# Optimization experiments

Measured on AMD Instinct MI355X. Metric: run time of the kernel, lower is better.

The kernel has to match this reference:

```python
import jax, jax.numpy as jnp
import numpy as np

N = 100000
E = 1600000
F_IN = 512
H1, C1 = 8, 8      # layer-1: 8 heads, 8 dims each (concat -> 64)
H2, C2 = 1, 16     # layer-2: 1 head, num_classes=16
SLOPE = 0.2        # GATConv leaky_relu negative slope


def setup_inputs() -> dict:
    key = jax.random.key(0)
    ks = jax.random.split(key, 10)
    x = jax.random.normal(ks[0], (N, F_IN), dtype=jnp.float32)
    edge_index = jax.random.randint(ks[1], (2, E), 0, N, dtype=jnp.int32)
    s = 0.05
    W1 = jax.random.normal(ks[2], (F_IN, H1 * C1), dtype=jnp.float32) * s
    a1_src = jax.random.normal(ks[3], (H1, C1), dtype=jnp.float32) * s
    a1_dst = jax.random.normal(ks[4], (H1, C1), dtype=jnp.float32) * s
    b1 = jnp.zeros((H1 * C1,), dtype=jnp.float32)
    W2 = jax.random.normal(ks[5], (H1 * C1, H2 * C2), dtype=jnp.float32) * s
    a2_src = jax.random.normal(ks[6], (H2, C2), dtype=jnp.float32) * s
    a2_dst = jax.random.normal(ks[7], (H2, C2), dtype=jnp.float32) * s
    b2 = jnp.zeros((H2 * C2,), dtype=jnp.float32)
    return {"x": x, "edge_index": edge_index, "W1": W1, "a1_src": a1_src,
            "a1_dst": a1_dst, "b1": b1, "W2": W2, "a2_src": a2_src,
            "a2_dst": a2_dst, "b2": b2}


def _gat_conv(h, src, dst, W, a_src, a_dst, b, heads, ch):
    n = h.shape[0]
    hp = (h @ W).reshape(n, heads, ch)                      # [N,H,C]
    al_s = jnp.einsum('nhc,hc->nh', hp, a_src)              # [N,H]
    al_d = jnp.einsum('nhc,hc->nh', hp, a_dst)              # [N,H]
    e = jax.nn.leaky_relu(al_s[src] + al_d[dst], SLOPE)     # [E,H]
    # segment softmax over edges sharing a destination (self-loops guarantee >=1 edge/node)
    emax = jax.lax.stop_gradient(jax.ops.segment_max(e, dst, num_segments=n))
    ee = jnp.exp(e - emax[dst])
    denom = jax.ops.segment_sum(ee, dst, num_segments=n)
    alpha = ee / denom[dst]                                 # [E,H]
    msg = hp[src] * alpha[:, :, None]                       # [E,H,C]
    out = jax.ops.segment_sum(msg, dst, num_segments=n)     # [N,H,C]
    return out.reshape(n, heads * ch) + b


def reference(x, edge_index, W1, a1_src, a1_dst, b1, W2, a2_src, a2_dst, b2):
    n = x.shape[0]
    loops = jnp.arange(n, dtype=edge_index.dtype)           # add_self_loops=True
    src = jnp.concatenate([edge_index[0], loops])
    dst = jnp.concatenate([edge_index[1], loops])
    h = jax.nn.elu(_gat_conv(x, src, dst, W1, a1_src, a1_dst, b1, H1, C1))
    h = _gat_conv(h, src, dst, W2, a2_src, a2_dst, b2, H2, C2)
    return jax.nn.log_softmax(h, axis=1)
```

## Files before the change

### kernel.cpp

```cpp
#include <hip/hip_runtime.h>
#include <hip/hip_bf16.h>

#define N_NODES 100000
#define F_IN    512
#define H1      8
#define C1      8
#define D1      64
#define C2      16
#define SLOPE   0.2f
#define CAP     48
#define PSHIFT  9
#define PPART   196
#define CAPP    9216
#define CHUNK   4096

typedef __bf16 bf16_t;
typedef bf16_t bf16x8 __attribute__((ext_vector_type(8)));
typedef float  f32x4  __attribute__((ext_vector_type(4)));

__global__ __launch_bounds__(256) void part_kernel(
    const float* __restrict__ W1, bf16_t* __restrict__ W1b,
    const int* __restrict__ ei, int* __restrict__ pcnt, int2* __restrict__ pfifo,
    int E, int total)
{
    __shared__ int hist[PPART];
    __shared__ int lofs[PPART];
    __shared__ int gbase[PPART];
    __shared__ int cursor[PPART];
    __shared__ int sdata[256];
    __shared__ int2 fifo[CHUNK];

    const int t = threadIdx.x;
    const int chunk0 = (int)blockIdx.x * CHUNK;

    for (int i = (int)blockIdx.x * 256 + t; i < 64 * 512; i += (int)gridDim.x * 256) {
        int nn = i >> 9, k = i & 511;
        W1b[i] = (bf16_t)W1[k * 64 + nn];
    }

    for (int i = t; i < PPART; i += 256) hist[i] = 0;
    __syncthreads();

    int srcs[16], dsts[16];
    const int e0 = chunk0 + t * 16;
    if (e0 + 16 <= E) {
#pragma unroll
        for (int q = 0; q < 4; ++q) {
            int4 s = *(const int4*)(ei + e0 + q * 4);
            int4 d = *(const int4*)(ei + E + e0 + q * 4);
            srcs[q*4+0]=s.x; srcs[q*4+1]=s.y; srcs[q*4+2]=s.z; srcs[q*4+3]=s.w;
            dsts[q*4+0]=d.x; dsts[q*4+1]=d.y; dsts[q*4+2]=d.z; dsts[q*4+3]=d.w;
        }
    } else {
#pragma unroll
        for (int j = 0; j < 16; ++j) {
            int e = e0 + j;
            if (e < E)          { srcs[j] = ei[e]; dsts[j] = ei[E + e]; }
            else if (e < total) { srcs[j] = dsts[j] = e - E; }
            else                { srcs[j] = -1;    dsts[j] = -1; }
        }
    }
#pragma unroll
    for (int j = 0; j < 16; ++j)
        if (dsts[j] >= 0) atomicAdd(&hist[dsts[j] >> PSHIFT], 1);
    __syncthreads();

    int hv = (t < PPART) ? hist[t] : 0;
    sdata[t] = hv;
    __syncthreads();
    for (int off = 1; off < 256; off <<= 1) {
        int x = (t >= off) ? sdata[t - off] : 0;
        __syncthreads();
        sdata[t] += x;
        __syncthreads();
    }
    if (t < PPART) {
        int lo = sdata[t] - hv;
        lofs[t]   = lo;
        cursor[t] = lo;
        gbase[t]  = hv ? atomicAdd(&pcnt[t], hv) : 0;
    }
    __syncthreads();

#pragma unroll
    for (int j = 0; j < 16; ++j) {
        if (dsts[j] >= 0) {
            int p = dsts[j] >> PSHIFT;
            int slot = atomicAdd(&cursor[p], 1);
            fifo[slot] = make_int2(srcs[j], dsts[j]);
        }
    }
    __syncthreads();

    const int w = t >> 6, lane = t & 63;
    for (int p = w; p < PPART; p += 4) {
        int len = hist[p];
        int lo  = lofs[p];
        int gb  = gbase[p];
        int2* dstp = pfifo + (size_t)p * CAPP;
        for (int j = lane; j < len; j += 64) {
            int g = gb + j;
            if (g < CAPP) dstp[g] = fifo[lo + j];
        }
    }
}

__global__ __launch_bounds__(512) void place_kernel(
    const int2* __restrict__ pfifo, const int* __restrict__ pcnt,
    int* __restrict__ buckets, int* __restrict__ cnt, int n)
{
    __shared__ int lcnt[1 << PSHIFT];
    const int p = blockIdx.x;
    const int dbase = p << PSHIFT;
    const int nd = min(1 << PSHIFT, n - dbase);
    const int t = threadIdx.x;
    for (int i = t; i < nd; i += 512) lcnt[i] = 0;
    __syncthreads();

    int len = pcnt[p]; if (len > CAPP) len = CAPP;
    const int2* f = pfifo + (size_t)p * CAPP;

    int i = t;
    for (; i + 1536 < len; i += 2048) {
        int2 e0 = f[i], e1 = f[i + 512], e2 = f[i + 1024], e3 = f[i + 1536];
        int s0 = atomicAdd(&lcnt[e0.y - dbase], 1);
        int s1 = atomicAdd(&lcnt[e1.y - dbase], 1);
        int s2 = atomicAdd(&lcnt[e2.y - dbase], 1);
        int s3 = atomicAdd(&lcnt[e3.y - dbase], 1);
        if (s0 < CAP) buckets[(size_t)e0.y * CAP + s0] = e0.x;
        if (s1 < CAP) buckets[(size_t)e1.y * CAP + s1] = e1.x;
        if (s2 < CAP) buckets[(size_t)e2.y * CAP + s2] = e2.x;
        if (s3 < CAP) buckets[(size_t)e3.y * CAP + s3] = e3.x;
    }
    for (; i < len; i += 512) {
        int2 e = f[i];
        int s = atomicAdd(&lcnt[e.y - dbase], 1);
        if (s < CAP) buckets[(size_t)e.y * CAP + s] = e.x;
    }
    __syncthreads();
    for (int i2 = t; i2 < nd; i2 += 512) cnt[dbase + i2] = min(lcnt[i2], CAP);
}

__global__ __launch_bounds__(512, 4) void gemm1_kernel(
    const float* __restrict__ X, const bf16_t* __restrict__ Bt,
    const float* __restrict__ a1s, const float* __restrict__ a1d,
    bf16_t* __restrict__ HPb, float* __restrict__ als1, float* __restrict__ ald1,
    int n)
{
    __shared__ __align__(16) bf16_t Bsm[8 * 4 * 64 * 8];

    const int t = threadIdx.x;
    const int rowbase = (int)blockIdx.x * 128;
    const int w = t >> 6;
    const int lane = t & 63;

    const int rloc = lane & 15;
    const int koff = (lane >> 4) * 8;

    int grow = rowbase + w * 16 + rloc;
    int growc = (grow < n) ? grow : (n - 1);
    const float* arow = X + (size_t)growc * F_IN + koff;

    f32x4 acc[4];
#pragma unroll
    for (int nt = 0; nt < 4; ++nt) acc[nt] = (f32x4){0.f, 0.f, 0.f, 0.f};

#pragma unroll
    for (int half = 0; half < 2; ++half) {
        for (int i = t; i < 2048; i += 512) {
            int l9 = i & 63;
            int nt = (i >> 6) & 3;
            int ks = i >> 8;
            int row = nt * 16 + (l9 & 15);
            int col = (half * 8 + ks) * 32 + (l9 >> 4) * 8;
            *(bf16x8*)(Bsm + (size_t)i * 8) =
                *(const bf16x8*)(Bt + (size_t)row * F_IN + col);
        }
        __syncthreads();

#pragma unroll 4
        for (int ks = 0; ks < 8; ++ks) {
            int kg = (half * 8 + ks) * 32;
            float4 xa0 = *(const float4*)(arow + kg);
            float4 xa1 = *(const float4*)(arow + kg + 4);
            bf16x8 af;
            af[0]=(bf16_t)xa0.x; af[1]=(bf16_t)xa0.y; af[2]=(bf16_t)xa0.z; af[3]=(bf16_t)xa0.w;
            af[4]=(bf16_t)xa1.x; af[5]=(bf16_t)xa1.y; af[6]=(bf16_t)xa1.z; af[7]=(bf16_t)xa1.w;
#pragma unroll
            for (int nt = 0; nt < 4; ++nt) {
                bf16x8 b = *(const bf16x8*)(Bsm + ((ks * 4 + nt) * 64 + lane) * 8);
                acc[nt] = __builtin_amdgcn_mfma_f32_16x16x32_bf16(af, b, acc[nt], 0, 0, 0);
            }
        }
        __syncthreads();
    }

    const int colg = lane & 15;
    const int quad = lane >> 4;
    const int b    = colg >> 3;
    float cs[4], cd[4];
#pragma unroll
    for (int nt = 0; nt < 4; ++nt) {
        cs[nt] = a1s[nt * 16 + colg];
        cd[nt] = a1d[nt * 16 + colg];
    }

#pragma unroll
    for (int i = 0; i < 4; ++i) {
        int r = rowbase + w * 16 + quad * 4 + i;
        bool ok = r < n;
        if (ok) {
            bf16_t* hr = HPb + (size_t)r * D1;
            hr[colg]      = (bf16_t)acc[0][i];
            hr[16 + colg] = (bf16_t)acc[1][i];
            hr[32 + colg] = (bf16_t)acc[2][i];
            hr[48 + colg] = (bf16_t)acc[3][i];
        }
#pragma unroll
        for (int nt = 0; nt < 4; ++nt) {
            float ps = acc[nt][i] * cs[nt];
            float pd = acc[nt][i] * cd[nt];
            ps += __shfl_xor(ps, 1, 64);  pd += __shfl_xor(pd, 1, 64);
            ps += __shfl_xor(ps, 2, 64);  pd += __shfl_xor(pd, 2, 64);
            ps += __shfl_xor(ps, 4, 64);  pd += __shfl_xor(pd, 4, 64);
            if (ok && (colg & 7) == 0) {
                als1[(size_t)r * 8 + 2 * nt + b] = ps;
                ald1[(size_t)r * 8 + 2 * nt + b] = pd;
            }
        }
    }
}

__global__ __launch_bounds__(256) void agg1_kernel(
    const bf16_t* __restrict__ hp1,
    const float* __restrict__ als, const float* __restrict__ ald,
    const int* __restrict__ cnt, const int* __restrict__ buckets,
    const float* __restrict__ b1,
    const float* __restrict__ W2,
    const float* __restrict__ a2s, const float* __restrict__ a2d,
    bf16_t* __restrict__ HP2b, float* __restrict__ als2, float* __restrict__ ald2,
    int n)
{
    __shared__ float Wsm[64 * 17];
    const int t = threadIdx.x;
    for (int i = t; i < 1024; i += 256)
        Wsm[(i >> 4) * 17 + (i & 15)] = W2[i];
    __syncthreads();

    int node = blockIdx.x * 4 + (t >> 6);
    if (node >= n) return;
    int lane = t & 63;
    int h = lane >> 3;

    int m = cnt[node]; if (m > CAP) m = CAP;
    const int* bp = buckets + (size_t)node * CAP;
    float ad = ald[node * 8 + h];
    float den = 0.f, acc = 0.f;

    int i = 0;
    for (; i + 8 <= m; i += 8) {
        int s0 = bp[i + 0], s1 = bp[i + 1], s2 = bp[i + 2], s3 = bp[i + 3];
        int s4 = bp[i + 4], s5 = bp[i + 5], s6 = bp[i + 6], s7 = bp[i + 7];
        float a0 = als[s0 * 8 + h], a1 = als[s1 * 8 + h];
        float a2 = als[s2 * 8 + h], a3 = als[s3 * 8 + h];
        float a4 = als[s4 * 8 + h], a5 = als[s5 * 8 + h];
        float a6 = als[s6 * 8 + h], a7 = als[s7 * 8 + h];
        float v0 = (float)hp1[(size_t)s0 * D1 + lane];
        float v1 = (float)hp1[(size_t)s1 * D1 + lane];
        float v2 = (float)hp1[(size_t)s2 * D1 + lane];
        float v3 = (float)hp1[(size_t)s3 * D1 + lane];
        float v4 = (float)hp1[(size_t)s4 * D1 + lane];
        float v5 = (float)hp1[(size_t)s5 * D1 + lane];
        float v6 = (float)hp1[(size_t)s6 * D1 + lane];
        float v7 = (float)hp1[(size_t)s7 * D1 + lane];
        float e0 = a0 + ad; e0 = (e0 > 0.f) ? e0 : SLOPE * e0;
        float e1 = a1 + ad; e1 = (e1 > 0.f) ? e1 : SLOPE * e1;
        float e2 = a2 + ad; e2 = (e2 > 0.f) ? e2 : SLOPE * e2;
        float e3 = a3 + ad; e3 = (e3 > 0.f) ? e3 : SLOPE * e3;
        float e4 = a4 + ad; e4 = (e4 > 0.f) ? e4 : SLOPE * e4;
        float e5 = a5 + ad; e5 = (e5 > 0.f) ? e5 : SLOPE * e5;
        float e6 = a6 + ad; e6 = (e6 > 0.f) ? e6 : SLOPE * e6;
        float e7 = a7 + ad; e7 = (e7 > 0.f) ? e7 : SLOPE * e7;
        float w0 = __expf(e0), w1 = __expf(e1), w2 = __expf(e2), w3 = __expf(e3);
        float w4 = __expf(e4), w5 = __expf(e5), w6 = __expf(e6), w7 = __expf(e7);
        den += ((w0 + w1) + (w2 + w3)) + ((w4 + w5) + (w6 + w7));
        acc = fmaf(w0, v0, acc);
        acc = fmaf(w1, v1, acc);
        acc = fmaf(w2, v2, acc);
        acc = fmaf(w3, v3, acc);
        acc = fmaf(w4, v4, acc);
        acc = fmaf(w5, v5, acc);
        acc = fmaf(w6, v6, acc);
        acc = fmaf(w7, v7, acc);
    }
    for (; i < m; ++i) {
        int s = bp[i];
        float e = als[s * 8 + h] + ad;
        e = (e > 0.f) ? e : SLOPE * e;
        float ee = __expf(e);
        den += ee;
        acc = fmaf(ee, (float)hp1[(size_t)s * D1 + lane], acc);
    }
    float v = acc / den + b1[lane];
    v = (v > 0.f) ? v : (__expf(v) - 1.f);

    const int g = lane >> 4, c = lane & 15;
    float o = 0.f;
#pragma unroll
    for (int kk = 0; kk < 16; ++kk) {
        float hk = __shfl(v, g * 16 + kk, 64);
        o = fmaf(hk, Wsm[(g * 16 + kk) * 17 + c], o);
    }
    o += __shfl_xor(o, 16, 64);
    o += __shfl_xor(o, 32, 64);
    if (g == 0) HP2b[(size_t)node * 16 + c] = (bf16_t)o;

    float rs = o * a2s[c];
    float rd = o * a2d[c];
    rs += __shfl_xor(rs, 1, 64);  rd += __shfl_xor(rd, 1, 64);
    rs += __shfl_xor(rs, 2, 64);  rd += __shfl_xor(rd, 2, 64);
    rs += __shfl_xor(rs, 4, 64);  rd += __shfl_xor(rd, 4, 64);
    rs += __shfl_xor(rs, 8, 64);  rd += __shfl_xor(rd, 8, 64);
    if (lane == 0) { als2[node] = rs; ald2[node] = rd; }
}

__global__ __launch_bounds__(256) void agg2_kernel(
    const bf16_t* __restrict__ hp2,
    const float* __restrict__ als, const float* __restrict__ ald,
    const int* __restrict__ cnt, const int* __restrict__ buckets,
    const float* __restrict__ b2,
    float* __restrict__ out, int n)
{
    int node = blockIdx.x * 16 + (threadIdx.x >> 4);
    if (node >= n) return;
    int c = threadIdx.x & 15;

    int m0c = cnt[node]; if (m0c > CAP) m0c = CAP;
    const int* bp = buckets + (size_t)node * CAP;
    float ad = ald[node];
    float den = 0.f, acc = 0.f;

    int i = 0;
    for (; i + 8 <= m0c; i += 8) {
        int s0 = bp[i + 0], s1 = bp[i + 1], s2 = bp[i + 2], s3 = bp[i + 3];
        int s4 = bp[i + 4], s5 = bp[i + 5], s6 = bp[i + 6], s7 = bp[i + 7];
        float a0 = als[s0], a1 = als[s1], a2 = als[s2], a3 = als[s3];
        float a4 = als[s4], a5 = als[s5], a6 = als[s6], a7 = als[s7];
        float v0 = (float)hp2[(size_t)s0 * 16 + c];
        float v1 = (float)hp2[(size_t)s1 * 16 + c];
        float v2 = (float)hp2[(size_t)s2 * 16 + c];
        float v3 = (float)hp2[(size_t)s3 * 16 + c];
        float v4 = (float)hp2[(size_t)s4 * 16 + c];
        float v5 = (float)hp2[(size_t)s5 * 16 + c];
        float v6 = (float)hp2[(size_t)s6 * 16 + c];
        float v7 = (float)hp2[(size_t)s7 * 16 + c];
        float e0 = a0 + ad; e0 = (e0 > 0.f) ? e0 : SLOPE * e0;
        float e1 = a1 + ad; e1 = (e1 > 0.f) ? e1 : SLOPE * e1;
        float e2 = a2 + ad; e2 = (e2 > 0.f) ? e2 : SLOPE * e2;
        float e3 = a3 + ad; e3 = (e3 > 0.f) ? e3 : SLOPE * e3;
        float e4 = a4 + ad; e4 = (e4 > 0.f) ? e4 : SLOPE * e4;
        float e5 = a5 + ad; e5 = (e5 > 0.f) ? e5 : SLOPE * e5;
        float e6 = a6 + ad; e6 = (e6 > 0.f) ? e6 : SLOPE * e6;
        float e7 = a7 + ad; e7 = (e7 > 0.f) ? e7 : SLOPE * e7;
        float w0 = __expf(e0), w1 = __expf(e1), w2 = __expf(e2), w3 = __expf(e3);
        float w4 = __expf(e4), w5 = __expf(e5), w6 = __expf(e6), w7 = __expf(e7);
        den += ((w0 + w1) + (w2 + w3)) + ((w4 + w5) + (w6 + w7));
        acc = fmaf(w0, v0, acc);
        acc = fmaf(w1, v1, acc);
        acc = fmaf(w2, v2, acc);
        acc = fmaf(w3, v3, acc);
        acc = fmaf(w4, v4, acc);
        acc = fmaf(w5, v5, acc);
        acc = fmaf(w6, v6, acc);
        acc = fmaf(w7, v7, acc);
    }
    for (; i < m0c; ++i) {
        int s = bp[i];
        float e = als[s] + ad;
        e = (e > 0.f) ? e : SLOPE * e;
        float ee = __expf(e);
        den += ee;
        acc = fmaf(ee, (float)hp2[(size_t)s * 16 + c], acc);
    }
    float v = acc / den + b2[c];

    float m = v;
    m = fmaxf(m, __shfl_xor(m, 8, 16));
    m = fmaxf(m, __shfl_xor(m, 4, 16));
    m = fmaxf(m, __shfl_xor(m, 2, 16));
    m = fmaxf(m, __shfl_xor(m, 1, 16));
    float ex = __expf(v - m);
    float sum = ex;
    sum += __shfl_xor(sum, 8, 16);
    sum += __shfl_xor(sum, 4, 16);
    sum += __shfl_xor(sum, 2, 16);
    sum += __shfl_xor(sum, 1, 16);
    out[(size_t)node * 16 + c] = v - m - __logf(sum);
}

extern "C" void kernel_launch(void* const* d_in, const int* in_sizes, int n_in,
                              void* d_out, int out_size, void* d_ws, size_t ws_size,
                              hipStream_t stream)
{
    const float* x      = (const float*)d_in[0];
    const int*   ei     = (const int*)  d_in[1];
    const float* W1     = (const float*)d_in[2];
    const float* a1_src = (const float*)d_in[3];
    const float* a1_dst = (const float*)d_in[4];
    const float* b1     = (const float*)d_in[5];
    const float* W2     = (const float*)d_in[6];
    const float* a2_src = (const float*)d_in[7];
    const float* a2_dst = (const float*)d_in[8];
    const float* b2     = (const float*)d_in[9];
    float* out = (float*)d_out;

    const int N = in_sizes[0] / F_IN;
    const int E = in_sizes[1] / 2;
    const int TOT = E + N;

    char* base = (char*)d_ws;
    size_t off = 0;
    auto carve = [&](size_t bytes) -> char* {
        char* p = base + off;
        off += (bytes + 255) & ~(size_t)255;
        return p;
    };
    bf16_t* hp1b    = (bf16_t*)carve((size_t)N * D1 * 2);
    float*  h1      = (float*) carve((size_t)N * D1 * 4);
    bf16_t* hp2b    = (bf16_t*)carve((size_t)N * 16 * 2);
    float*  als1    = (float*) carve((size_t)N * 8 * 4);
    float*  ald1    = (float*) carve((size_t)N * 8 * 4);
    float*  als2    = (float*) carve((size_t)N * 4);
    float*  ald2    = (float*) carve((size_t)N * 4);
    int*    cnt     = (int*)   carve((size_t)N * 4);
    int*    pcnt    = (int*)   carve((size_t)PPART * 4);
    int*    buckets = (int*)   carve((size_t)N * CAP * 4);
    bf16_t* W1b     = (bf16_t*)carve((size_t)64 * 512 * 2);
    int2*  pfifo   = (int2*)h1;

    const int Gp = (TOT + CHUNK - 1) / CHUNK;

    hipMemsetAsync(pcnt, 0, (size_t)PPART * 4, stream);

    part_kernel<<<Gp, 256, 0, stream>>>(W1, W1b, ei, pcnt, pfifo, E, TOT);
    place_kernel<<<PPART, 512, 0, stream>>>(pfifo, pcnt, buckets, cnt, N);

    gemm1_kernel<<<(N + 127) / 128, 512, 0, stream>>>(x, W1b, a1_src, a1_dst,
                                                      hp1b, als1, ald1, N);

    agg1_kernel<<<(N + 3) / 4, 256, 0, stream>>>(hp1b, als1, ald1, cnt, buckets,
                                                 b1, W2, a2_src, a2_dst,
                                                 hp2b, als2, ald2, N);

    agg2_kernel<<<(N + 15) / 16, 256, 0, stream>>>(hp2b, als2, ald2, cnt, buckets, b2, out, N);
}
```

Before: 507.9 us.

## Merge place and GEMM kernels into one launch; split agg1 edges across wave pairs

The bucket placement work and the layer-1 GEMM now share a single launch, with the first PPART blocks doing placement and the rest doing GEMM rows. The two independent stages can then overlap on the GPU, and one launch gap goes away. agg1 now uses 512 threads, with two waves per node splitting the 8-edge groups and combining partial sums through shared memory. This doubles memory-level parallelism for the gather at the cost of a block-wide sync and shared-memory traffic, and the merged kernel's shared-memory footprint rises.

```diff
diff --git a/kernel.cpp b/kernel.cpp
--- a/kernel.cpp
+++ b/kernel.cpp
@@ -105,52 +105,52 @@
     }
 }
 
-__global__ __launch_bounds__(512) void place_kernel(
+__global__ __launch_bounds__(512, 4) void pg_kernel(
     const int2* __restrict__ pfifo, const int* __restrict__ pcnt,
-    int* __restrict__ buckets, int* __restrict__ cnt, int n)
-{
-    __shared__ int lcnt[1 << PSHIFT];
-    const int p = blockIdx.x;
-    const int dbase = p << PSHIFT;
-    const int nd = min(1 << PSHIFT, n - dbase);
-    const int t = threadIdx.x;
-    for (int i = t; i < nd; i += 512) lcnt[i] = 0;
-    __syncthreads();
-
-    int len = pcnt[p]; if (len > CAPP) len = CAPP;
-    const int2* f = pfifo + (size_t)p * CAPP;
-
-    int i = t;
-    for (; i + 1536 < len; i += 2048) {
-        int2 e0 = f[i], e1 = f[i + 512], e2 = f[i + 1024], e3 = f[i + 1536];
-        int s0 = atomicAdd(&lcnt[e0.y - dbase], 1);
-        int s1 = atomicAdd(&lcnt[e1.y - dbase], 1);
-        int s2 = atomicAdd(&lcnt[e2.y - dbase], 1);
-        int s3 = atomicAdd(&lcnt[e3.y - dbase], 1);
-        if (s0 < CAP) buckets[(size_t)e0.y * CAP + s0] = e0.x;
-        if (s1 < CAP) buckets[(size_t)e1.y * CAP + s1] = e1.x;
-        if (s2 < CAP) buckets[(size_t)e2.y * CAP + s2] = e2.x;
-        if (s3 < CAP) buckets[(size_t)e3.y * CAP + s3] = e3.x;
-    }
-    for (; i < len; i += 512) {
-        int2 e = f[i];
-        int s = atomicAdd(&lcnt[e.y - dbase], 1);
-        if (s < CAP) buckets[(size_t)e.y * CAP + s] = e.x;
-    }
-    __syncthreads();
-    for (int i2 = t; i2 < nd; i2 += 512) cnt[dbase + i2] = min(lcnt[i2], CAP);
-}
-
-__global__ __launch_bounds__(512, 4) void gemm1_kernel(
+    int* __restrict__ buckets, int* __restrict__ cnt,
     const float* __restrict__ X, const bf16_t* __restrict__ Bt,
     const float* __restrict__ a1s, const float* __restrict__ a1d,
     bf16_t* __restrict__ HPb, float* __restrict__ als1, float* __restrict__ ald1,
     int n)
 {
+    __shared__ int lcnt[1 << PSHIFT];
     __shared__ __align__(16) bf16_t Bsm[8 * 4 * 64 * 8];
 
     const int t = threadIdx.x;
-    const int rowbase = (int)blockIdx.x * 128;
+
+    if (blockIdx.x < PPART) {
+        const int p = blockIdx.x;
+        const int dbase = p << PSHIFT;
+        const int nd = min(1 << PSHIFT, n - dbase);
+        for (int i = t; i < nd; i += 512) lcnt[i] = 0;
+        __syncthreads();
+
+        int len = pcnt[p]; if (len > CAPP) len = CAPP;
+        const int2* f = pfifo + (size_t)p * CAPP;
+
+        int i = t;
+        for (; i + 1536 < len; i += 2048) {
+            int2 e0 = f[i], e1 = f[i + 512], e2 = f[i + 1024], e3 = f[i + 1536];
+            int s0 = atomicAdd(&lcnt[e0.y - dbase], 1);
+            int s1 = atomicAdd(&lcnt[e1.y - dbase], 1);
+            int s2 = atomicAdd(&lcnt[e2.y - dbase], 1);
+            int s3 = atomicAdd(&lcnt[e3.y - dbase], 1);
+            if (s0 < CAP) buckets[(size_t)e0.y * CAP + s0] = e0.x;
+            if (s1 < CAP) buckets[(size_t)e1.y * CAP + s1] = e1.x;
+            if (s2 < CAP) buckets[(size_t)e2.y * CAP + s2] = e2.x;
+            if (s3 < CAP) buckets[(size_t)e3.y * CAP + s3] = e3.x;
+        }
+        for (; i < len; i += 512) {
+            int2 e = f[i];
+            int s = atomicAdd(&lcnt[e.y - dbase], 1);
+            if (s < CAP) buckets[(size_t)e.y * CAP + s] = e.x;
+        }
+        __syncthreads();
+        for (int i2 = t; i2 < nd; i2 += 512) cnt[dbase + i2] = min(lcnt[i2], CAP);
+        return;
+    }
+
+    const int rowbase = ((int)blockIdx.x - PPART) * 128;
     const int w = t >> 6;
     const int lane = t & 63;
 
@@ -231,7 +231,7 @@
     }
 }
 
-__global__ __launch_bounds__(256) void agg1_kernel(
+__global__ __launch_bounds__(512) void agg1_kernel(
     const bf16_t* __restrict__ hp1,
     const float* __restrict__ als, const float* __restrict__ ald,
     const int* __restrict__ cnt, const int* __restrict__ buckets,
@@ -242,25 +242,33 @@
     int n)
 {
     __shared__ float Wsm[64 * 17];
+    __shared__ float sacc[8][64];
+    __shared__ float sden[8][64];
+
     const int t = threadIdx.x;
-    for (int i = t; i < 1024; i += 256)
+    for (int i = t; i < 1024; i += 512)
         Wsm[(i >> 4) * 17 + (i & 15)] = W2[i];
-    __syncthreads();
-
-    int node = blockIdx.x * 4 + (t >> 6);
-    if (node >= n) return;
-    int lane = t & 63;
-    int h = lane >> 3;
-
-    int m = cnt[node]; if (m > CAP) m = CAP;
-    const int* bp = buckets + (size_t)node * CAP;
-    float ad = ald[node * 8 + h];
+
+    const int wv   = t >> 6;
+    const int pair = wv & 1;
+    const int slot = wv >> 1;
+    const int lane = t & 63;
+    const int h    = lane >> 3;
+
+    int node  = blockIdx.x * 4 + slot;
+    bool valid = node < n;
+    int nodec = valid ? node : (n - 1);
+
+    int m = cnt[nodec]; if (m > CAP) m = CAP;
+    const int* bp = buckets + (size_t)nodec * CAP;
+    float ad = ald[nodec * 8 + h];
     float den = 0.f, acc = 0.f;
 
-    int i = 0;
-    for (; i + 8 <= m; i += 8) {
-        int s0 = bp[i + 0], s1 = bp[i + 1], s2 = bp[i + 2], s3 = bp[i + 3];
-        int s4 = bp[i + 4], s5 = bp[i + 5], s6 = bp[i + 6], s7 = bp[i + 7];
+    const int G = m >> 3;
+    for (int g = pair; g < G; g += 2) {
+        const int base = g * 8;
+        int s0 = bp[base + 0], s1 = bp[base + 1], s2 = bp[base + 2], s3 = bp[base + 3];
+        int s4 = bp[base + 4], s5 = bp[base + 5], s6 = bp[base + 6], s7 = bp[base + 7];
         float a0 = als[s0 * 8 + h], a1 = als[s1 * 8 + h];
         float a2 = als[s2 * 8 + h], a3 = als[s3 * 8 + h];
         float a4 = als[s4 * 8 + h], a5 = als[s5 * 8 + h];
@@ -293,35 +301,46 @@
         acc = fmaf(w6, v6, acc);
         acc = fmaf(w7, v7, acc);
     }
-    for (; i < m; ++i) {
-        int s = bp[i];
-        float e = als[s * 8 + h] + ad;
-        e = (e > 0.f) ? e : SLOPE * e;
-        float ee = __expf(e);
-        den += ee;
-        acc = fmaf(ee, (float)hp1[(size_t)s * D1 + lane], acc);
-    }
-    float v = acc / den + b1[lane];
-    v = (v > 0.f) ? v : (__expf(v) - 1.f);
-
-    const int g = lane >> 4, c = lane & 15;
-    float o = 0.f;
-#pragma unroll
-    for (int kk = 0; kk < 16; ++kk) {
-        float hk = __shfl(v, g * 16 + kk, 64);
-        o = fmaf(hk, Wsm[(g * 16 + kk) * 17 + c], o);
-    }
-    o += __shfl_xor(o, 16, 64);
-    o += __shfl_xor(o, 32, 64);
-    if (g == 0) HP2b[(size_t)node * 16 + c] = (bf16_t)o;
-
-    float rs = o * a2s[c];
-    float rd = o * a2d[c];
-    rs += __shfl_xor(rs, 1, 64);  rd += __shfl_xor(rd, 1, 64);
-    rs += __shfl_xor(rs, 2, 64);  rd += __shfl_xor(rd, 2, 64);
-    rs += __shfl_xor(rs, 4, 64);  rd += __shfl_xor(rd, 4, 64);
-    rs += __shfl_xor(rs, 8, 64);  rd += __shfl_xor(rd, 8, 64);
-    if (lane == 0) { als2[node] = rs; ald2[node] = rd; }
+    if (pair == (G & 1)) {
+        for (int i = G * 8; i < m; ++i) {
+            int s = bp[i];
+            float e = als[s * 8 + h] + ad;
+            e = (e > 0.f) ? e : SLOPE * e;
+            float ee = __expf(e);
+            den += ee;
+            acc = fmaf(ee, (float)hp1[(size_t)s * D1 + lane], acc);
+        }
+    }
+
+    sacc[wv][lane] = acc;
+    sden[wv][lane] = den;
+    __syncthreads();
+
+    if (pair == 0) {
+        acc += sacc[wv ^ 1][lane];
+        den += sden[wv ^ 1][lane];
+        float v = acc / den + b1[lane];
+        v = (v > 0.f) ? v : (__expf(v) - 1.f);
+
+        const int g2 = lane >> 4, c = lane & 15;
+        float o = 0.f;
+#pragma unroll
+        for (int kk = 0; kk < 16; ++kk) {
+            float hk = __shfl(v, g2 * 16 + kk, 64);
+            o = fmaf(hk, Wsm[(g2 * 16 + kk) * 17 + c], o);
+        }
+        o += __shfl_xor(o, 16, 64);
+        o += __shfl_xor(o, 32, 64);
+        if (valid && g2 == 0) HP2b[(size_t)node * 16 + c] = (bf16_t)o;
+
+        float rs = o * a2s[c];
+        float rd = o * a2d[c];
+        rs += __shfl_xor(rs, 1, 64);  rd += __shfl_xor(rd, 1, 64);
+        rs += __shfl_xor(rs, 2, 64);  rd += __shfl_xor(rd, 2, 64);
+        rs += __shfl_xor(rs, 4, 64);  rd += __shfl_xor(rd, 4, 64);
+        rs += __shfl_xor(rs, 8, 64);  rd += __shfl_xor(rd, 8, 64);
+        if (valid && lane == 0) { als2[node] = rs; ald2[node] = rd; }
+    }
 }
 
 __global__ __launch_bounds__(256) void agg2_kernel(
@@ -439,16 +458,17 @@
     int2*  pfifo   = (int2*)h1;
 
     const int Gp = (TOT + CHUNK - 1) / CHUNK;
+    const int Gg = (N + 127) / 128;
 
     hipMemsetAsync(pcnt, 0, (size_t)PPART * 4, stream);
 
     part_kernel<<<Gp, 256, 0, stream>>>(W1, W1b, ei, pcnt, pfifo, E, TOT);
-    place_kernel<<<PPART, 512, 0, stream>>>(pfifo, pcnt, buckets, cnt, N);
-
-    gemm1_kernel<<<(N + 127) / 128, 512, 0, stream>>>(x, W1b, a1_src, a1_dst,
-                                                      hp1b, als1, ald1, N);
-
-    agg1_kernel<<<(N + 3) / 4, 256, 0, stream>>>(hp1b, als1, ald1, cnt, buckets,
+
+    pg_kernel<<<PPART + Gg, 512, 0, stream>>>(pfifo, pcnt, buckets, cnt,
+                                              x, W1b, a1_src, a1_dst,
+                                              hp1b, als1, ald1, N);
+
+    agg1_kernel<<<(N + 3) / 4, 512, 0, stream>>>(hp1b, als1, ald1, cnt, buckets,
                                                  b1, W2, a2_src, a2_dst,
                                                  hp2b, als2, ald2, N);
 
```

Result: slower. 588.1 us (+15.8%).

## Fuse bucket placement with GEMM1 launch and batch-gather aggregation neighbors

Applied to the files above, without the earlier changes.

Merges place_kernel and gemm1_kernel into one launch. The first PPART blocks do the bucket placement and the remaining blocks do the GEMM, so the placement work can overlap the GEMM and one launch gap goes away. The two aggregation kernels now load all 48 bucket indices with vector int4 loads into registers. They then issue 16 independent gathers per section, masking out-of-range edges, which raises memory-level parallelism. This costs more registers (the occupancy hint is set to 6) and adds wasted gathers of node 0 for padded slots.

```diff
diff --git a/kernel.cpp b/kernel.cpp
--- a/kernel.cpp
+++ b/kernel.cpp
@@ -105,52 +105,52 @@
     }
 }
 
-__global__ __launch_bounds__(512) void place_kernel(
+__global__ __launch_bounds__(512, 4) void pg_kernel(
     const int2* __restrict__ pfifo, const int* __restrict__ pcnt,
-    int* __restrict__ buckets, int* __restrict__ cnt, int n)
-{
-    __shared__ int lcnt[1 << PSHIFT];
-    const int p = blockIdx.x;
-    const int dbase = p << PSHIFT;
-    const int nd = min(1 << PSHIFT, n - dbase);
-    const int t = threadIdx.x;
-    for (int i = t; i < nd; i += 512) lcnt[i] = 0;
-    __syncthreads();
-
-    int len = pcnt[p]; if (len > CAPP) len = CAPP;
-    const int2* f = pfifo + (size_t)p * CAPP;
-
-    int i = t;
-    for (; i + 1536 < len; i += 2048) {
-        int2 e0 = f[i], e1 = f[i + 512], e2 = f[i + 1024], e3 = f[i + 1536];
-        int s0 = atomicAdd(&lcnt[e0.y - dbase], 1);
-        int s1 = atomicAdd(&lcnt[e1.y - dbase], 1);
-        int s2 = atomicAdd(&lcnt[e2.y - dbase], 1);
-        int s3 = atomicAdd(&lcnt[e3.y - dbase], 1);
-        if (s0 < CAP) buckets[(size_t)e0.y * CAP + s0] = e0.x;
-        if (s1 < CAP) buckets[(size_t)e1.y * CAP + s1] = e1.x;
-        if (s2 < CAP) buckets[(size_t)e2.y * CAP + s2] = e2.x;
-        if (s3 < CAP) buckets[(size_t)e3.y * CAP + s3] = e3.x;
-    }
-    for (; i < len; i += 512) {
-        int2 e = f[i];
-        int s = atomicAdd(&lcnt[e.y - dbase], 1);
-        if (s < CAP) buckets[(size_t)e.y * CAP + s] = e.x;
-    }
-    __syncthreads();
-    for (int i2 = t; i2 < nd; i2 += 512) cnt[dbase + i2] = min(lcnt[i2], CAP);
-}
-
-__global__ __launch_bounds__(512, 4) void gemm1_kernel(
+    int* __restrict__ buckets, int* __restrict__ cnt,
     const float* __restrict__ X, const bf16_t* __restrict__ Bt,
     const float* __restrict__ a1s, const float* __restrict__ a1d,
     bf16_t* __restrict__ HPb, float* __restrict__ als1, float* __restrict__ ald1,
     int n)
 {
+    __shared__ int lcnt[1 << PSHIFT];
     __shared__ __align__(16) bf16_t Bsm[8 * 4 * 64 * 8];
 
     const int t = threadIdx.x;
-    const int rowbase = (int)blockIdx.x * 128;
+
+    if (blockIdx.x < PPART) {
+        const int p = blockIdx.x;
+        const int dbase = p << PSHIFT;
+        const int nd = min(1 << PSHIFT, n - dbase);
+        for (int i = t; i < nd; i += 512) lcnt[i] = 0;
+        __syncthreads();
+
+        int len = pcnt[p]; if (len > CAPP) len = CAPP;
+        const int2* f = pfifo + (size_t)p * CAPP;
+
+        int i = t;
+        for (; i + 1536 < len; i += 2048) {
+            int2 e0 = f[i], e1 = f[i + 512], e2 = f[i + 1024], e3 = f[i + 1536];
+            int s0 = atomicAdd(&lcnt[e0.y - dbase], 1);
+            int s1 = atomicAdd(&lcnt[e1.y - dbase], 1);
+            int s2 = atomicAdd(&lcnt[e2.y - dbase], 1);
+            int s3 = atomicAdd(&lcnt[e3.y - dbase], 1);
+            if (s0 < CAP) buckets[(size_t)e0.y * CAP + s0] = e0.x;
+            if (s1 < CAP) buckets[(size_t)e1.y * CAP + s1] = e1.x;
+            if (s2 < CAP) buckets[(size_t)e2.y * CAP + s2] = e2.x;
+            if (s3 < CAP) buckets[(size_t)e3.y * CAP + s3] = e3.x;
+        }
+        for (; i < len; i += 512) {
+            int2 e = f[i];
+            int s = atomicAdd(&lcnt[e.y - dbase], 1);
+            if (s < CAP) buckets[(size_t)e.y * CAP + s] = e.x;
+        }
+        __syncthreads();
+        for (int i2 = t; i2 < nd; i2 += 512) cnt[dbase + i2] = min(lcnt[i2], CAP);
+        return;
+    }
+
+    const int rowbase = ((int)blockIdx.x - PPART) * 128;
     const int w = t >> 6;
     const int lane = t & 63;
 
@@ -231,7 +231,27 @@
     }
 }
 
-__global__ __launch_bounds__(256) void agg1_kernel(
+#define AGG1_SEC(G0)                                                        \
+    {                                                                       \
+        float a_[16], v_[16];                                               \
+        _Pragma("unroll")                                                   \
+        for (int j = 0; j < 16; ++j) {                                      \
+            int s = (G0 + j < m) ? idx[G0 + j] : 0;                         \
+            a_[j] = als[s * 8 + h];                                         \
+            v_[j] = (float)hp1[(size_t)s * D1 + lane];                      \
+        }                                                                   \
+        _Pragma("unroll")                                                   \
+        for (int j = 0; j < 16; ++j) {                                      \
+            float e = a_[j] + ad;                                           \
+            e = (e > 0.f) ? e : SLOPE * e;                                  \
+            float wgt = __expf(e);                                          \
+            if (G0 + j >= m) wgt = 0.f;                                     \
+            den += wgt;                                                     \
+            acc = fmaf(wgt, v_[j], acc);                                    \
+        }                                                                   \
+    }
+
+__global__ __launch_bounds__(256, 6) void agg1_kernel(
     const bf16_t* __restrict__ hp1,
     const float* __restrict__ als, const float* __restrict__ ald,
     const int* __restrict__ cnt, const int* __restrict__ buckets,
@@ -255,65 +275,32 @@
     int m = cnt[node]; if (m > CAP) m = CAP;
     const int* bp = buckets + (size_t)node * CAP;
     float ad = ald[node * 8 + h];
+
+    int idx[48];
+#pragma unroll
+    for (int q = 0; q < 12; ++q) {
+        int4 v4 = *(const int4*)(bp + q * 4);
+        idx[q*4+0] = v4.x; idx[q*4+1] = v4.y; idx[q*4+2] = v4.z; idx[q*4+3] = v4.w;
+    }
+
     float den = 0.f, acc = 0.f;
-
-    int i = 0;
-    for (; i + 8 <= m; i += 8) {
-        int s0 = bp[i + 0], s1 = bp[i + 1], s2 = bp[i + 2], s3 = bp[i + 3];
-        int s4 = bp[i + 4], s5 = bp[i + 5], s6 = bp[i + 6], s7 = bp[i + 7];
-        float a0 = als[s0 * 8 + h], a1 = als[s1 * 8 + h];
-        float a2 = als[s2 * 8 + h], a3 = als[s3 * 8 + h];
-        float a4 = als[s4 * 8 + h], a5 = als[s5 * 8 + h];
-        float a6 = als[s6 * 8 + h], a7 = als[s7 * 8 + h];
-        float v0 = (float)hp1[(size_t)s0 * D1 + lane];
-        float v1 = (float)hp1[(size_t)s1 * D1 + lane];
-        float v2 = (float)hp1[(size_t)s2 * D1 + lane];
-        float v3 = (float)hp1[(size_t)s3 * D1 + lane];
-        float v4 = (float)hp1[(size_t)s4 * D1 + lane];
-        float v5 = (float)hp1[(size_t)s5 * D1 + lane];
-        float v6 = (float)hp1[(size_t)s6 * D1 + lane];
-        float v7 = (float)hp1[(size_t)s7 * D1 + lane];
-        float e0 = a0 + ad; e0 = (e0 > 0.f) ? e0 : SLOPE * e0;
-        float e1 = a1 + ad; e1 = (e1 > 0.f) ? e1 : SLOPE * e1;
-        float e2 = a2 + ad; e2 = (e2 > 0.f) ? e2 : SLOPE * e2;
-        float e3 = a3 + ad; e3 = (e3 > 0.f) ? e3 : SLOPE * e3;
-        float e4 = a4 + ad; e4 = (e4 > 0.f) ? e4 : SLOPE * e4;
-        float e5 = a5 + ad; e5 = (e5 > 0.f) ? e5 : SLOPE * e5;
-        float e6 = a6 + ad; e6 = (e6 > 0.f) ? e6 : SLOPE * e6;
-        float e7 = a7 + ad; e7 = (e7 > 0.f) ? e7 : SLOPE * e7;
-        float w0 = __expf(e0), w1 = __expf(e1), w2 = __expf(e2), w3 = __expf(e3);
-        float w4 = __expf(e4), w5 = __expf(e5), w6 = __expf(e6), w7 = __expf(e7);
-        den += ((w0 + w1) + (w2 + w3)) + ((w4 + w5) + (w6 + w7));
-        acc = fmaf(w0, v0, acc);
-        acc = fmaf(w1, v1, acc);
-        acc = fmaf(w2, v2, acc);
-        acc = fmaf(w3, v3, acc);
-        acc = fmaf(w4, v4, acc);
-        acc = fmaf(w5, v5, acc);
-        acc = fmaf(w6, v6, acc);
-        acc = fmaf(w7, v7, acc);
-    }
-    for (; i < m; ++i) {
-        int s = bp[i];
-        float e = als[s * 8 + h] + ad;
-        e = (e > 0.f) ? e : SLOPE * e;
-        float ee = __expf(e);
-        den += ee;
-        acc = fmaf(ee, (float)hp1[(size_t)s * D1 + lane], acc);
-    }
+    AGG1_SEC(0);
+    if (m > 16) AGG1_SEC(16);
+    if (m > 32) AGG1_SEC(32);
+
     float v = acc / den + b1[lane];
     v = (v > 0.f) ? v : (__expf(v) - 1.f);
 
-    const int g = lane >> 4, c = lane & 15;
+    const int g2 = lane >> 4, c = lane & 15;
     float o = 0.f;
 #pragma unroll
     for (int kk = 0; kk < 16; ++kk) {
-        float hk = __shfl(v, g * 16 + kk, 64);
-        o = fmaf(hk, Wsm[(g * 16 + kk) * 17 + c], o);
+        float hk = __shfl(v, g2 * 16 + kk, 64);
+        o = fmaf(hk, Wsm[(g2 * 16 + kk) * 17 + c], o);
     }
     o += __shfl_xor(o, 16, 64);
     o += __shfl_xor(o, 32, 64);
-    if (g == 0) HP2b[(size_t)node * 16 + c] = (bf16_t)o;
+    if (g2 == 0) HP2b[(size_t)node * 16 + c] = (bf16_t)o;
 
     float rs = o * a2s[c];
     float rd = o * a2d[c];
@@ -324,7 +311,27 @@
     if (lane == 0) { als2[node] = rs; ald2[node] = rd; }
 }
 
-__global__ __launch_bounds__(256) void agg2_kernel(
+#define AGG2_SEC(G0)                                                        \
+    {                                                                       \
+        float a_[16], v_[16];                                               \
+        _Pragma("unroll")                                                   \
+        for (int j = 0; j < 16; ++j) {                                      \
+            int s = (G0 + j < m) ? idx[G0 + j] : 0;                         \
+            a_[j] = als[s];                                                 \
+            v_[j] = (float)hp2[(size_t)s * 16 + c];                         \
+        }                                                                   \
+        _Pragma("unroll")                                                   \
+        for (int j = 0; j < 16; ++j) {                                      \
+            float e = a_[j] + ad;                                           \
+            e = (e > 0.f) ? e : SLOPE * e;                                  \
+            float wgt = __expf(e);                                          \
+            if (G0 + j >= m) wgt = 0.f;                                     \
+            den += wgt;                                                     \
+            acc = fmaf(wgt, v_[j], acc);                                    \
+        }                                                                   \
+    }
+
+__global__ __launch_bounds__(256, 6) void agg2_kernel(
     const bf16_t* __restrict__ hp2,
     const float* __restrict__ als, const float* __restrict__ ald,
     const int* __restrict__ cnt, const int* __restrict__ buckets,
@@ -335,67 +342,36 @@
     if (node >= n) return;
     int c = threadIdx.x & 15;
 
-    int m0c = cnt[node]; if (m0c > CAP) m0c = CAP;
+    int m = cnt[node]; if (m > CAP) m = CAP;
     const int* bp = buckets + (size_t)node * CAP;
     float ad = ald[node];
+
+    int idx[48];
+#pragma unroll
+    for (int q = 0; q < 12; ++q) {
+        int4 v4 = *(const int4*)(bp + q * 4);
+        idx[q*4+0] = v4.x; idx[q*4+1] = v4.y; idx[q*4+2] = v4.z; idx[q*4+3] = v4.w;
+    }
+
     float den = 0.f, acc = 0.f;
-
-    int i = 0;
-    for (; i + 8 <= m0c; i += 8) {
-        int s0 = bp[i + 0], s1 = bp[i + 1], s2 = bp[i + 2], s3 = bp[i + 3];
-        int s4 = bp[i + 4], s5 = bp[i + 5], s6 = bp[i + 6], s7 = bp[i + 7];
-        float a0 = als[s0], a1 = als[s1], a2 = als[s2], a3 = als[s3];
-        float a4 = als[s4], a5 = als[s5], a6 = als[s6], a7 = als[s7];
-        float v0 = (float)hp2[(size_t)s0 * 16 + c];
-        float v1 = (float)hp2[(size_t)s1 * 16 + c];
-        float v2 = (float)hp2[(size_t)s2 * 16 + c];
-        float v3 = (float)hp2[(size_t)s3 * 16 + c];
-        float v4 = (float)hp2[(size_t)s4 * 16 + c];
-        float v5 = (float)hp2[(size_t)s5 * 16 + c];
-        float v6 = (float)hp2[(size_t)s6 * 16 + c];
-        float v7 = (float)hp2[(size_t)s7 * 16 + c];
-        float e0 = a0 + ad; e0 = (e0 > 0.f) ? e0 : SLOPE * e0;
-        float e1 = a1 + ad; e1 = (e1 > 0.f) ? e1 : SLOPE * e1;
-        float e2 = a2 + ad; e2 = (e2 > 0.f) ? e2 : SLOPE * e2;
-        float e3 = a3 + ad; e3 = (e3 > 0.f) ? e3 : SLOPE * e3;
-        float e4 = a4 + ad; e4 = (e4 > 0.f) ? e4 : SLOPE * e4;
-        float e5 = a5 + ad; e5 = (e5 > 0.f) ? e5 : SLOPE * e5;
-        float e6 = a6 + ad; e6 = (e6 > 0.f) ? e6 : SLOPE * e6;
-        float e7 = a7 + ad; e7 = (e7 > 0.f) ? e7 : SLOPE * e7;
-        float w0 = __expf(e0), w1 = __expf(e1), w2 = __expf(e2), w3 = __expf(e3);
-        float w4 = __expf(e4), w5 = __expf(e5), w6 = __expf(e6), w7 = __expf(e7);
-        den += ((w0 + w1) + (w2 + w3)) + ((w4 + w5) + (w6 + w7));
-        acc = fmaf(w0, v0, acc);
-        acc = fmaf(w1, v1, acc);
-        acc = fmaf(w2, v2, acc);
-        acc = fmaf(w3, v3, acc);
-        acc = fmaf(w4, v4, acc);
-        acc = fmaf(w5, v5, acc);
-        acc = fmaf(w6, v6, acc);
-        acc = fmaf(w7, v7, acc);
-    }
-    for (; i < m0c; ++i) {
-        int s = bp[i];
-        float e = als[s] + ad;
-        e = (e > 0.f) ? e : SLOPE * e;
-        float ee = __expf(e);
-        den += ee;
-        acc = fmaf(ee, (float)hp2[(size_t)s * 16 + c], acc);
-    }
+    AGG2_SEC(0);
+    if (m > 16) AGG2_SEC(16);
+    if (m > 32) AGG2_SEC(32);
+
     float v = acc / den + b2[c];
 
-    float m = v;
-    m = fmaxf(m, __shfl_xor(m, 8, 16));
-    m = fmaxf(m, __shfl_xor(m, 4, 16));
-    m = fmaxf(m, __shfl_xor(m, 2, 16));
-    m = fmaxf(m, __shfl_xor(m, 1, 16));
-    float ex = __expf(v - m);
+    float mx = v;
+    mx = fmaxf(mx, __shfl_xor(mx, 8, 16));
+    mx = fmaxf(mx, __shfl_xor(mx, 4, 16));
+    mx = fmaxf(mx, __shfl_xor(mx, 2, 16));
+    mx = fmaxf(mx, __shfl_xor(mx, 1, 16));
+    float ex = __expf(v - mx);
     float sum = ex;
     sum += __shfl_xor(sum, 8, 16);
     sum += __shfl_xor(sum, 4, 16);
     sum += __shfl_xor(sum, 2, 16);
     sum += __shfl_xor(sum, 1, 16);
-    out[(size_t)node * 16 + c] = v - m - __logf(sum);
+    out[(size_t)node * 16 + c] = v - mx - __logf(sum);
 }
 
 extern "C" void kernel_launch(void* const* d_in, const int* in_sizes, int n_in,
@@ -439,14 +415,15 @@
     int2*  pfifo   = (int2*)h1;
 
     const int Gp = (TOT + CHUNK - 1) / CHUNK;
+    const int Gg = (N + 127) / 128;
 
     hipMemsetAsync(pcnt, 0, (size_t)PPART * 4, stream);
 
     part_kernel<<<Gp, 256, 0, stream>>>(W1, W1b, ei, pcnt, pfifo, E, TOT);
-    place_kernel<<<PPART, 512, 0, stream>>>(pfifo, pcnt, buckets, cnt, N);
-
-    gemm1_kernel<<<(N + 127) / 128, 512, 0, stream>>>(x, W1b, a1_src, a1_dst,
-                                                      hp1b, als1, ald1, N);
+
+    pg_kernel<<<PPART + Gg, 512, 0, stream>>>(pfifo, pcnt, buckets, cnt,
+                                              x, W1b, a1_src, a1_dst,
+                                              hp1b, als1, ald1, N);
 
     agg1_kernel<<<(N + 3) / 4, 256, 0, stream>>>(hp1b, als1, ald1, cnt, buckets,
                                                  b1, W2, a2_src, a2_dst,
```

Measured after the change: 523.4 us. +3.1%, slower.
